# Performance work log

Measured on AMD Instinct MI355X. Metric: run time of the kernel, lower is better.

The kernel has to match this reference:

```python
import jax, jax.numpy as jnp
import numpy as np
import functools

N_NODES = 16
WIDTH = 64
C_DIM = 3
LATENT_DIM = 8
B = 131072


def build_graph(n=N_NODES, k=4, p=0.75, seed=0):
    """Watts-Strogatz-style random graph oriented low->high node id (DAG),
    mirroring build_random_graph(nodes, 1 input, 1 output, p=0.75, k=4)."""
    rng = np.random.RandomState(seed)
    edges = set()
    for i in range(n):
        for d in range(1, k // 2 + 1):
            j = (i + d) % n
            if rng.rand() < p:
                j = int(rng.randint(n))
            a, b = min(i, j), max(i, j)
            if a != b:
                edges.add((a, b))
    preds = [set() for _ in range(n)]
    for a, b in edges:
        preds[b].add(a)
    # every non-source node must have a predecessor (connectivity)
    for j in range(1, n):
        if not preds[j]:
            a = int(rng.randint(j))
            preds[j].add(a)
            edges.add((a, j))
    succs = [set() for _ in range(n)]
    for a, b in edges:
        succs[a].add(b)
    preds = [sorted(p_) for p_ in preds]
    sources = [j for j in range(n) if not preds[j]]   # receive the INR feature f
    sinks = [j for j in range(n) if not succs[j]]     # combined into the single output
    return preds, sources, sinks


def gaussian(x):
    return jnp.exp(-0.5 * x * x)

# 'large' activation set for graph nodes, assigned deterministically per node
GRAPH_ACTS = [jnp.tanh, jax.nn.elu, jax.nn.softplus, jnp.sin, gaussian]


def setup_inputs() -> dict:
    key = jax.random.key(0)
    ks = jax.random.split(key, 16)

    def nrm(k, shape, s):
        return jax.random.normal(k, shape, dtype=jnp.float32) * s

    inputs = jax.random.normal(ks[0], (B, 3, 1), dtype=jnp.float32)   # (x, y, r) coords
    latents = jax.random.normal(ks[1], (B, LATENT_DIM), dtype=jnp.float32)
    Wl = nrm(ks[2], (WIDTH, LATENT_DIM), 0.3)
    bl = jnp.zeros((WIDTH,), jnp.float32)
    Wx = nrm(ks[3], (WIDTH, 1), 1.0)
    Wy = nrm(ks[4], (WIDTH, 1), 1.0)
    Wr = nrm(ks[5], (WIDTH, 1), 1.0)
    W1 = nrm(ks[6], (WIDTH, WIDTH), 0.15)
    b1 = jnp.zeros((WIDTH,), jnp.float32)
    gW = nrm(ks[7], (N_NODES, WIDTH, WIDTH), 0.15)   # per-graph-node Linear(width,width)
    gB = jnp.zeros((N_NODES, WIDTH), jnp.float32)
    outW = nrm(ks[8], (C_DIM, WIDTH), 0.15)          # combine -> c_dim output
    outb = jnp.zeros((C_DIM,), jnp.float32)
    scale = jnp.ones((1,), jnp.float32)              # ScaleAct learnable scalar
    return {"inputs": inputs, "latents": latents, "Wl": Wl, "bl": bl, "Wx": Wx,
            "Wy": Wy, "Wr": Wr, "W1": W1, "b1": b1, "gW": gW, "gB": gB,
            "outW": outW, "outb": outb, "scale": scale}


def reference(inputs, latents, Wl, bl, Wx, Wy, Wr, W1, b1, gW, gB, outW, outb, scale):
    x, y, r = inputs[:, 0, :], inputs[:, 1, :], inputs[:, 2, :]   # each (B, 1)
    latents_ = jnp.tanh(latents @ Wl.T + bl)      # acts_start[0] = Tanh
    r_ = jax.nn.elu(r @ Wr.T)                     # acts_start[1] = ELU
    y_ = jax.nn.softplus(y @ Wy.T)                # acts_start[2] = Softplus
    x_ = jnp.tanh(x @ Wx.T)                       # acts_start[3] = Tanh
    f = gaussian(x_ + y_ + r_ + latents_)         # acts_start[4] = Gaussian
    f = jnp.sin(f @ W1.T + b1)                    # acts_start[5] = SinLayer

    # random-topology graph network: gather(sum preds) -> linear -> activation
    preds, sources, sinks = build_graph()
    hs = []
    for j in range(N_NODES):
        if j in sources:
            inp = f
        else:
            inp = functools.reduce(lambda a, b_: a + b_, [hs[i] for i in preds[j]])
        hs.append(GRAPH_ACTS[j % len(GRAPH_ACTS)](inp @ gW[j].T + gB[j]))
    agg = functools.reduce(lambda a, b_: a + b_, [hs[j] for j in sinks])
    res = (agg @ outW.T + outb) * scale           # combine + ScaleAct
    return jax.nn.sigmoid(res)                    # final_activation='sigmoid'
```

## Files before the change

### kernel.cpp

```cpp
#include <hip/hip_runtime.h>
#include <cstdint>

#define NN 16
#define W64 64
#define MT 64
#define NSTAGE 17
#define IST 72
#define WST 68

typedef _Float16 half8   __attribute__((ext_vector_type(8)));
typedef _Float16 half16  __attribute__((ext_vector_type(16)));
typedef float    floatx4 __attribute__((ext_vector_type(4)));

struct GPlan {
    unsigned pred[NN];
    unsigned sinkmask;
    int slot[NSTAGE];
    int nslot;
};

constexpr unsigned mt_next(unsigned (&mt)[624], int &mti) {
    if (mti >= 624) {
        for (int i = 0; i < 624; ++i) {
            const unsigned y = (mt[i] & 0x80000000u) | (mt[(i + 1) % 624] & 0x7fffffffu);
            unsigned v = mt[(i + 397) % 624] ^ (y >> 1);
            if (y & 1u) v ^= 0x9908b0dfu;
            mt[i] = v;
        }
        mti = 0;
    }
    unsigned y = mt[mti++];
    y ^= y >> 11;
    y ^= (y << 7)  & 0x9d2c5680u;
    y ^= (y << 15) & 0xefc60000u;
    y ^= y >> 18;
    return y;
}
constexpr double mt_rnd(unsigned (&mt)[624], int &mti) {
    const unsigned a = mt_next(mt, mti) >> 5;
    const unsigned b = mt_next(mt, mti) >> 6;
    return (a * 67108864.0 + b) / 9007199254740992.0;
}
constexpr long mt_randint(unsigned (&mt)[624], int &mti, long n) {
    const unsigned long maxv = (unsigned long)n - 1;
    if (maxv == 0) return 0;
    unsigned long mask = maxv;
    mask |= mask >> 1;  mask |= mask >> 2;  mask |= mask >> 4;
    mask |= mask >> 8;  mask |= mask >> 16;
    unsigned long v = (unsigned long)mt_next(mt, mti) & mask;
    while (v > maxv) v = (unsigned long)mt_next(mt, mti) & mask;
    return (long)v;
}

constexpr GPlan build_plan() {
    GPlan P = {};
    unsigned mt[624] = {};
    mt[0] = 0u;
    for (int i = 1; i < 624; ++i)
        mt[i] = 1812433253u * (mt[i-1] ^ (mt[i-1] >> 30)) + (unsigned)i;
    int mti = 624;

    bool edge[NN][NN] = {};
    for (int i = 0; i < NN; ++i) {
        for (int d = 1; d <= 2; ++d) {
            int j = (i + d) & (NN - 1);
            if (mt_rnd(mt, mti) < 0.75) j = (int)mt_randint(mt, mti, NN);
            const int a = i < j ? i : j;
            const int b = i < j ? j : i;
            if (a != b) edge[a][b] = true;
        }
    }
    for (int a = 0; a < NN; ++a)
        for (int b = 0; b < NN; ++b)
            if (edge[a][b]) P.pred[b] |= 1u << a;
    for (int j = 1; j < NN; ++j) {
        if (!P.pred[j]) {
            const int a = (int)mt_randint(mt, mti, j);
            P.pred[j] |= 1u << a;
            edge[a][j] = true;
        }
    }
    unsigned succ[NN] = {};
    for (int a = 0; a < NN; ++a)
        for (int b = 0; b < NN; ++b)
            if (edge[a][b]) succ[a] |= 1u << b;
    for (int j = 0; j < NN; ++j)
        if (!succ[j]) P.sinkmask |= 1u << j;

    int lastuse[NSTAGE] = {};
    for (int v = 0; v < NSTAGE; ++v) lastuse[v] = -1;
    for (int j = 0; j < NN; ++j) {
        const unsigned pm = P.pred[j];
        if (pm == 0u) { if (j > lastuse[16]) lastuse[16] = j; }
        else for (int i = 0; i < NN; ++i)
            if (pm & (1u << i)) { if (j > lastuse[i]) lastuse[i] = j; }
    }
    for (int i = 0; i < NN; ++i)
        if (P.sinkmask & (1u << i)) lastuse[i] = 17;

    int defstage[NSTAGE] = {};
    for (int i = 0; i < NN; ++i) defstage[i] = i + 1;
    defstage[16] = 0;

    int nmax = 0;
    for (int s = 0; s <= 16; ++s) {
        const int w = (s == 0) ? 16 : (s - 1);
        bool busy[NSTAGE] = {};
        for (int v = 0; v < NSTAGE; ++v) {
            if (v == w) continue;
            if (defstage[v] < s && lastuse[v] >= s)
                busy[P.slot[v]] = true;
        }
        int k = 0;
        while (busy[k]) ++k;
        P.slot[w] = k;
        if (k + 1 > nmax) nmax = k + 1;
    }
    P.nslot = nmax;
    return P;
}

constexpr GPlan kPlan = build_plan();
constexpr int NSLOT = kPlan.nslot;

__device__ __forceinline__ float act_tanh(float x)     { return 1.0f - 2.0f / (1.0f + __expf(2.0f * x)); }
__device__ __forceinline__ float act_elu(float x)      { return x > 0.0f ? x : __expf(x) - 1.0f; }
__device__ __forceinline__ float act_softplus(float x) { return fmaxf(x, 0.0f) + __logf(1.0f + __expf(-fabsf(x))); }
__device__ __forceinline__ float act_gauss(float x)    { return __expf(-0.5f * x * x); }

__device__ __forceinline__ float apply_act(int a, float x) {
    switch (a) {
        case 0:  return act_tanh(x);
        case 1:  return act_elu(x);
        case 2:  return act_softplus(x);
        case 3:  return __sinf(x);
        default: return act_gauss(x);
    }
}

__device__ __forceinline__ half8 cvt8(float4 a, float4 b) {
    half8 h;
    h[0]=(_Float16)a.x; h[1]=(_Float16)a.y; h[2]=(_Float16)a.z; h[3]=(_Float16)a.w;
    h[4]=(_Float16)b.x; h[5]=(_Float16)b.y; h[6]=(_Float16)b.z; h[7]=(_Float16)b.w;
    return h;
}

__global__ void convert_weights(const float* __restrict__ W1,
                                const float* __restrict__ gW,
                                _Float16* __restrict__ ws)
{
    const int i = blockIdx.x * 256 + threadIdx.x;
    if (i >= NSTAGE * 4096) return;
    const float v = (i < 4096) ? W1[i] : gW[i - 4096];
    ws[i] = (_Float16)v;
}

template<bool F16W>
__global__ __launch_bounds__(256, 3) void inr_mfma_kernel(
    const float* __restrict__ inputs, const float* __restrict__ latents,
    const float* __restrict__ Wl, const float* __restrict__ bl,
    const float* __restrict__ Wx, const float* __restrict__ Wy,
    const float* __restrict__ Wr, const float* __restrict__ W1,
    const float* __restrict__ b1, const float* __restrict__ gW,
    const float* __restrict__ gB, const float* __restrict__ outW,
    const float* __restrict__ outb, const float* __restrict__ scale,
    const _Float16* __restrict__ wsW,
    float* __restrict__ out, int Btot)
{
    __shared__ __align__(16) _Float16 inpbuf[2][MT * IST];
    __shared__ __align__(16) _Float16 wbuf[W64 * WST];

    const int tid  = threadIdx.x;
    const int lane = tid & 63;
    const int wv   = tid >> 6;
    const int q    = lane >> 4;
    const int c    = lane & 15;
    const int rowbase = wv * 16;
    const int m0   = blockIdx.x * MT;

    const int srow = tid >> 3;
    const int sc8  = tid & 7;

    half16 hreg[NSLOT];

    {
        const int em = tid >> 2, ep = tid & 3;
        int mg = m0 + em; if (mg >= Btot) mg = Btot - 1;
        const float x = inputs[mg * 3 + 0];
        const float y = inputs[mg * 3 + 1];
        const float r = inputs[mg * 3 + 2];
        const float4 l0 = *(const float4*)(latents + mg * 8);
        const float4 l1 = *(const float4*)(latents + mg * 8 + 4);
        #pragma unroll
        for (int i = 0; i < 16; ++i) {
            const int k = ep * 16 + i;
            const float4 a = *(const float4*)(Wl + k * 8);
            const float4 b = *(const float4*)(Wl + k * 8 + 4);
            float ld = bl[k];
            ld = fmaf(l0.x, a.x, ld); ld = fmaf(l0.y, a.y, ld);
            ld = fmaf(l0.z, a.z, ld); ld = fmaf(l0.w, a.w, ld);
            ld = fmaf(l1.x, b.x, ld); ld = fmaf(l1.y, b.y, ld);
            ld = fmaf(l1.z, b.z, ld); ld = fmaf(l1.w, b.w, ld);
            const float tk = act_tanh(x * Wx[k]) + act_softplus(y * Wy[k])
                           + act_elu(r * Wr[k]) + act_tanh(ld);
            inpbuf[0][em * IST + k] = (_Float16)act_gauss(tk);
        }
    }
    if constexpr (F16W) {
        const uint4* src = (const uint4*)wsW;
        const uint4 h0 = src[tid], h1 = src[tid + 256];
        *(uint4*)&wbuf[srow * WST + sc8 * 8]        = h0;
        *(uint4*)&wbuf[(srow + 32) * WST + sc8 * 8] = h1;
    } else {
        const float4* src = (const float4*)W1;
        const float4 f0 = src[2 * tid],       f1 = src[2 * tid + 1];
        const float4 f2 = src[2 * tid + 512], f3 = src[2 * tid + 513];
        *(half8*)&wbuf[srow * WST + sc8 * 8]        = cvt8(f0, f1);
        *(half8*)&wbuf[(srow + 32) * WST + sc8 * 8] = cvt8(f2, f3);
    }
    __syncthreads();

    #pragma unroll
    for (int s = 0; s < NSTAGE; ++s) {
        const int slot = s & 1;

        uint4  nh0 = {}, nh1 = {};
        float4 nf0 = {}, nf1 = {}, nf2 = {}, nf3 = {};
        if (s + 1 < NSTAGE) {
            if constexpr (F16W) {
                const uint4* src = (const uint4*)(wsW + (s + 1) * 4096);
                nh0 = src[tid]; nh1 = src[tid + 256];
            } else {
                const float4* src = (const float4*)(gW + s * 4096);
                nf0 = src[2 * tid];       nf1 = src[2 * tid + 1];
                nf2 = src[2 * tid + 512]; nf3 = src[2 * tid + 513];
            }
        }

        const half8 a0 = *(const half8*)&inpbuf[slot][(rowbase + c) * IST +  0 + q * 8];
        const half8 a1 = *(const half8*)&inpbuf[slot][(rowbase + c) * IST + 32 + q * 8];

        const float* bias = (s == 0) ? b1 : (gB + (s - 1) * W64);
        floatx4 acc[4];
        #pragma unroll
        for (int t = 0; t < 4; ++t) {
            const half8 b0  = *(const half8*)&wbuf[(t * 16 + c) * WST +  0 + q * 8];
            const half8 b1f = *(const half8*)&wbuf[(t * 16 + c) * WST + 32 + q * 8];
            const float bs = bias[t * 16 + c];
            floatx4 z = {bs, bs, bs, bs};
            z = __builtin_amdgcn_mfma_f32_16x16x32_f16(a0, b0, z, 0, 0, 0);
            z = __builtin_amdgcn_mfma_f32_16x16x32_f16(a1, b1f, z, 0, 0, 0);
            acc[t] = z;
        }

        const int an    = (s == 0) ? 3 : ((s - 1) % 5);
        const int hslot = kPlan.slot[(s == 0) ? 16 : (s - 1)];
        #pragma unroll
        for (int t = 0; t < 4; ++t) {
            #pragma unroll
            for (int r = 0; r < 4; ++r) {
                const float v = apply_act(an, acc[t][r]);
                hreg[hslot][t * 4 + r] = (_Float16)v;
            }
        }

        if (s + 1 < NSTAGE) {
            const unsigned pm = kPlan.pred[s];
            half16 sum;
            if (pm == 0u) {
                sum = hreg[kPlan.slot[16]];
            } else {
                #pragma unroll
                for (int v = 0; v < 16; ++v) sum[v] = (_Float16)0.0f;
                #pragma unroll
                for (int i = 0; i < NN; ++i) {
                    if (pm & (1u << i)) {
                        sum += hreg[kPlan.slot[i]];
                    }
                }
            }
            const int wslot = (s + 1) & 1;
            #pragma unroll
            for (int t = 0; t < 4; ++t)
                #pragma unroll
                for (int r = 0; r < 4; ++r)
                    inpbuf[wslot][(rowbase + q * 4 + r) * IST + t * 16 + c] =
                        sum[t * 4 + r];

            __syncthreads();
            if constexpr (F16W) {
                *(uint4*)&wbuf[srow * WST + sc8 * 8]        = nh0;
                *(uint4*)&wbuf[(srow + 32) * WST + sc8 * 8] = nh1;
            } else {
                *(half8*)&wbuf[srow * WST + sc8 * 8]        = cvt8(nf0, nf1);
                *(half8*)&wbuf[(srow + 32) * WST + sc8 * 8] = cvt8(nf2, nf3);
            }
            __syncthreads();
        }
    }

    {
        half16 sum;
        #pragma unroll
        for (int v = 0; v < 16; ++v) sum[v] = (_Float16)0.0f;
        #pragma unroll
        for (int j = 0; j < NN; ++j) {
            if (kPlan.sinkmask & (1u << j)) {
                sum += hreg[kPlan.slot[j]];
            }
        }
        #pragma unroll
        for (int t = 0; t < 4; ++t)
            #pragma unroll
            for (int r = 0; r < 4; ++r)
                inpbuf[1][(rowbase + q * 4 + r) * IST + t * 16 + c] = sum[t * 4 + r];
    }
    {
        const int em = tid >> 2, ep = tid & 3;
        float p0 = 0.f, p1 = 0.f, p2 = 0.f;
        #pragma unroll
        for (int h = 0; h < 2; ++h) {
            const half8 hv = *(const half8*)&inpbuf[1][em * IST + ep * 16 + h * 8];
            #pragma unroll
            for (int i = 0; i < 8; ++i) {
                const float av = (float)hv[i];
                const int k = ep * 16 + h * 8 + i;
                p0 = fmaf(av, outW[0 * W64 + k], p0);
                p1 = fmaf(av, outW[1 * W64 + k], p1);
                p2 = fmaf(av, outW[2 * W64 + k], p2);
            }
        }
        p0 += __shfl_xor(p0, 1); p0 += __shfl_xor(p0, 2);
        p1 += __shfl_xor(p1, 1); p1 += __shfl_xor(p1, 2);
        p2 += __shfl_xor(p2, 1); p2 += __shfl_xor(p2, 2);
        const int mg = m0 + em;
        if (ep < 3 && mg < Btot) {
            const float pr = (ep == 0) ? p0 : ((ep == 1) ? p1 : p2);
            const float res = (pr + outb[ep]) * scale[0];
            out[mg * 3 + ep] = 1.0f / (1.0f + __expf(-res));
        }
    }
}

extern "C" void kernel_launch(void* const* d_in, const int* in_sizes, int n_in,
                              void* d_out, int out_size, void* d_ws, size_t ws_size,
                              hipStream_t stream)
{
    const float* inputs  = (const float*)d_in[0];
    const float* latents = (const float*)d_in[1];
    const float* Wl      = (const float*)d_in[2];
    const float* bl      = (const float*)d_in[3];
    const float* Wx      = (const float*)d_in[4];
    const float* Wy      = (const float*)d_in[5];
    const float* Wr      = (const float*)d_in[6];
    const float* W1      = (const float*)d_in[7];
    const float* b1      = (const float*)d_in[8];
    const float* gW      = (const float*)d_in[9];
    const float* gB      = (const float*)d_in[10];
    const float* outW    = (const float*)d_in[11];
    const float* outb    = (const float*)d_in[12];
    const float* scale   = (const float*)d_in[13];
    float* out = (float*)d_out;

    const int Btot = in_sizes[0] / 3;
    const int blocks = (Btot + MT - 1) / MT;
    const size_t wbytes = (size_t)NSTAGE * 4096 * sizeof(_Float16);

    if (ws_size >= wbytes) {
        _Float16* wsW = (_Float16*)d_ws;
        convert_weights<<<(NSTAGE * 4096 + 255) / 256, 256, 0, stream>>>(W1, gW, wsW);
        inr_mfma_kernel<true><<<blocks, 256, 0, stream>>>(
            inputs, latents, Wl, bl, Wx, Wy, Wr, W1, b1, gW, gB, outW, outb, scale,
            wsW, out, Btot);
    } else {
        inr_mfma_kernel<false><<<blocks, 256, 0, stream>>>(
            inputs, latents, Wl, bl, Wx, Wy, Wr, W1, b1, gW, gB, outW, outb, scale,
            (const _Float16*)nullptr, out, Btot);
    }
}
```

Measured before the change: 181.7 us.

## Switch to 32x32x16 MFMA with 128-row tiles and single input buffer

Doubles the per-block row tile to 128 rows so each wave computes a 32x64 output using 32x32x16 f16 MFMAs instead of 16x16x32. Each loaded weight fragment now serves twice as many rows, which halves weight staging and barriers per sample. The double-buffered input tile becomes a single buffer with a narrower stride, and an explicit barrier is added before the output projection. The cost is twice the register state for hidden activations, which is why occupancy is lowered to 2 blocks, and less latency hiding.

```diff
diff --git a/kernel.cpp b/kernel.cpp
--- a/kernel.cpp
+++ b/kernel.cpp
@@ -3,14 +3,14 @@
 
 #define NN 16
 #define W64 64
-#define MT 64
+#define MT 128
 #define NSTAGE 17
-#define IST 72
+#define IST 68
 #define WST 68
 
-typedef _Float16 half8   __attribute__((ext_vector_type(8)));
-typedef _Float16 half16  __attribute__((ext_vector_type(16)));
-typedef float    floatx4 __attribute__((ext_vector_type(4)));
+typedef _Float16 half8    __attribute__((ext_vector_type(8)));
+typedef _Float16 half16   __attribute__((ext_vector_type(16)));
+typedef float    floatx16 __attribute__((ext_vector_type(16)));
 
 struct GPlan {
     unsigned pred[NN];
@@ -156,7 +156,7 @@
 }
 
 template<bool F16W>
-__global__ __launch_bounds__(256, 3) void inr_mfma_kernel(
+__global__ __launch_bounds__(256, 2) void inr_mfma_kernel(
     const float* __restrict__ inputs, const float* __restrict__ latents,
     const float* __restrict__ Wl, const float* __restrict__ bl,
     const float* __restrict__ Wx, const float* __restrict__ Wy,
@@ -167,24 +167,25 @@
     const _Float16* __restrict__ wsW,
     float* __restrict__ out, int Btot)
 {
-    __shared__ __align__(16) _Float16 inpbuf[2][MT * IST];
+    __shared__ __align__(16) _Float16 inpbuf[MT * IST];
     __shared__ __align__(16) _Float16 wbuf[W64 * WST];
 
     const int tid  = threadIdx.x;
     const int lane = tid & 63;
     const int wv   = tid >> 6;
-    const int q    = lane >> 4;
-    const int c    = lane & 15;
-    const int rowbase = wv * 16;
+    const int l31  = lane & 31;
+    const int hi   = lane >> 5;
+    const int rowbase = wv * 32;
     const int m0   = blockIdx.x * MT;
 
     const int srow = tid >> 3;
     const int sc8  = tid & 7;
 
-    half16 hreg[NSLOT];
-
-    {
-        const int em = tid >> 2, ep = tid & 3;
+    half16 hreg[NSLOT][2];
+
+    #pragma unroll
+    for (int hf = 0; hf < 2; ++hf) {
+        const int em = hf * 64 + (tid >> 2), ep = tid & 3;
         int mg = m0 + em; if (mg >= Btot) mg = Btot - 1;
         const float x = inputs[mg * 3 + 0];
         const float y = inputs[mg * 3 + 1];
@@ -203,7 +204,7 @@
             ld = fmaf(l1.z, b.z, ld); ld = fmaf(l1.w, b.w, ld);
             const float tk = act_tanh(x * Wx[k]) + act_softplus(y * Wy[k])
                            + act_elu(r * Wr[k]) + act_tanh(ld);
-            inpbuf[0][em * IST + k] = (_Float16)act_gauss(tk);
+            inpbuf[em * IST + k] = (_Float16)act_gauss(tk);
         }
     }
     if constexpr (F16W) {
@@ -222,8 +223,6 @@
 
     #pragma unroll
     for (int s = 0; s < NSTAGE; ++s) {
-        const int slot = s & 1;
-
         uint4  nh0 = {}, nh1 = {};
         float4 nf0 = {}, nf1 = {}, nf2 = {}, nf3 = {};
         if (s + 1 < NSTAGE) {
@@ -237,55 +236,62 @@
             }
         }
 
-        const half8 a0 = *(const half8*)&inpbuf[slot][(rowbase + c) * IST +  0 + q * 8];
-        const half8 a1 = *(const half8*)&inpbuf[slot][(rowbase + c) * IST + 32 + q * 8];
+        half8 afr[4];
+        #pragma unroll
+        for (int st = 0; st < 4; ++st)
+            afr[st] = *(const half8*)&inpbuf[(rowbase + l31) * IST + st * 16 + hi * 8];
 
         const float* bias = (s == 0) ? b1 : (gB + (s - 1) * W64);
-        floatx4 acc[4];
-        #pragma unroll
-        for (int t = 0; t < 4; ++t) {
-            const half8 b0  = *(const half8*)&wbuf[(t * 16 + c) * WST +  0 + q * 8];
-            const half8 b1f = *(const half8*)&wbuf[(t * 16 + c) * WST + 32 + q * 8];
-            const float bs = bias[t * 16 + c];
-            floatx4 z = {bs, bs, bs, bs};
-            z = __builtin_amdgcn_mfma_f32_16x16x32_f16(a0, b0, z, 0, 0, 0);
-            z = __builtin_amdgcn_mfma_f32_16x16x32_f16(a1, b1f, z, 0, 0, 0);
+        floatx16 acc[2];
+        #pragma unroll
+        for (int t = 0; t < 2; ++t) {
+            const float bs = bias[t * 32 + l31];
+            floatx16 z;
+            #pragma unroll
+            for (int v = 0; v < 16; ++v) z[v] = bs;
+            #pragma unroll
+            for (int st = 0; st < 4; ++st) {
+                const half8 bfr = *(const half8*)
+                    &wbuf[(t * 32 + l31) * WST + st * 16 + hi * 8];
+                z = __builtin_amdgcn_mfma_f32_32x32x16_f16(afr[st], bfr, z, 0, 0, 0);
+            }
             acc[t] = z;
         }
 
         const int an    = (s == 0) ? 3 : ((s - 1) % 5);
         const int hslot = kPlan.slot[(s == 0) ? 16 : (s - 1)];
         #pragma unroll
-        for (int t = 0; t < 4; ++t) {
-            #pragma unroll
-            for (int r = 0; r < 4; ++r) {
-                const float v = apply_act(an, acc[t][r]);
-                hreg[hslot][t * 4 + r] = (_Float16)v;
-            }
-        }
+        for (int t = 0; t < 2; ++t)
+            #pragma unroll
+            for (int v = 0; v < 16; ++v)
+                hreg[hslot][t][v] = (_Float16)apply_act(an, acc[t][v]);
 
         if (s + 1 < NSTAGE) {
             const unsigned pm = kPlan.pred[s];
-            half16 sum;
+            half16 sum[2];
             if (pm == 0u) {
-                sum = hreg[kPlan.slot[16]];
+                sum[0] = hreg[kPlan.slot[16]][0];
+                sum[1] = hreg[kPlan.slot[16]][1];
             } else {
                 #pragma unroll
-                for (int v = 0; v < 16; ++v) sum[v] = (_Float16)0.0f;
+                for (int t = 0; t < 2; ++t)
+                    #pragma unroll
+                    for (int v = 0; v < 16; ++v) sum[t][v] = (_Float16)0.0f;
                 #pragma unroll
                 for (int i = 0; i < NN; ++i) {
                     if (pm & (1u << i)) {
-                        sum += hreg[kPlan.slot[i]];
+                        sum[0] += hreg[kPlan.slot[i]][0];
+                        sum[1] += hreg[kPlan.slot[i]][1];
                     }
                 }
             }
-            const int wslot = (s + 1) & 1;
-            #pragma unroll
-            for (int t = 0; t < 4; ++t)
+            #pragma unroll
+            for (int t = 0; t < 2; ++t)
                 #pragma unroll
-                for (int r = 0; r < 4; ++r)
-                    inpbuf[wslot][(rowbase + q * 4 + r) * IST + t * 16 + c] =
-                        sum[t * 4 + r];
+                for (int v = 0; v < 16; ++v) {
+                    const int row = rowbase + (v & 3) + 8 * (v >> 2) + 4 * hi;
+                    inpbuf[row * IST + t * 32 + l31] = sum[t][v];
+                }
 
             __syncthreads();
             if constexpr (F16W) {
@@ -300,27 +306,34 @@
     }
 
     {
-        half16 sum;
-        #pragma unroll
-        for (int v = 0; v < 16; ++v) sum[v] = (_Float16)0.0f;
+        half16 sum[2];
+        #pragma unroll
+        for (int t = 0; t < 2; ++t)
+            #pragma unroll
+            for (int v = 0; v < 16; ++v) sum[t][v] = (_Float16)0.0f;
         #pragma unroll
         for (int j = 0; j < NN; ++j) {
             if (kPlan.sinkmask & (1u << j)) {
-                sum += hreg[kPlan.slot[j]];
-            }
-        }
-        #pragma unroll
-        for (int t = 0; t < 4; ++t)
-            #pragma unroll
-            for (int r = 0; r < 4; ++r)
-                inpbuf[1][(rowbase + q * 4 + r) * IST + t * 16 + c] = sum[t * 4 + r];
-    }
-    {
-        const int em = tid >> 2, ep = tid & 3;
+                sum[0] += hreg[kPlan.slot[j]][0];
+                sum[1] += hreg[kPlan.slot[j]][1];
+            }
+        }
+        #pragma unroll
+        for (int t = 0; t < 2; ++t)
+            #pragma unroll
+            for (int v = 0; v < 16; ++v) {
+                const int row = rowbase + (v & 3) + 8 * (v >> 2) + 4 * hi;
+                inpbuf[row * IST + t * 32 + l31] = sum[t][v];
+            }
+    }
+    __syncthreads();
+    #pragma unroll
+    for (int hf = 0; hf < 2; ++hf) {
+        const int em = hf * 64 + (tid >> 2), ep = tid & 3;
         float p0 = 0.f, p1 = 0.f, p2 = 0.f;
         #pragma unroll
         for (int h = 0; h < 2; ++h) {
-            const half8 hv = *(const half8*)&inpbuf[1][em * IST + ep * 16 + h * 8];
+            const half8 hv = *(const half8*)&inpbuf[em * IST + ep * 16 + h * 8];
             #pragma unroll
             for (int i = 0; i < 8; ++i) {
                 const float av = (float)hv[i];
```

Result: slower. 266.4 us (+46.6%).
